# Kernel optimization log

Hardware: AMD Instinct MI355X
Metric: run time of the kernel (lower is better)

The kernel has to match this reference:

```python
import jax, jax.numpy as jnp
import numpy as np

EPS = 1e-6  # kernel_epsilon
NUM_HEADS = 16
NUM_SCALES = 3
ROPE_BASE = 10000.0


def _rope(x, base=ROPE_BASE):
    # x: [B, S, N, D]; rotary applied along seq dim 1 (RotaryPositionEmbedding.forward)
    B, S, N, D = x.shape
    inv_freq = 1.0 / (base ** (jnp.arange(0, D, 2, dtype=jnp.float32) / D))  # [D/2]
    t = jnp.arange(S, dtype=jnp.float32)
    freqs = t[:, None] * inv_freq[None, :]            # [S, D/2]
    emb = jnp.concatenate([freqs, freqs], axis=-1)    # [S, D]
    cos = jnp.cos(emb)[None, :, None, :]
    sin = jnp.sin(emb)[None, :, None, :]
    x1, x2 = jnp.split(x, 2, axis=-1)
    rot = jnp.concatenate([-x2, x1], axis=-1)         # rotate_half
    return x * cos + rot * sin


def _kernel(x):
    # elu kernel: F.elu(x) + 1.0 + epsilon
    return jax.nn.elu(x) + 1.0 + EPS


def setup_inputs() -> dict:
    key = jax.random.key(0)
    ks = jax.random.split(key, 12)
    B, S, H = 4, 2048, 1024
    sc = 1.0 / np.sqrt(H)
    inp = {
        "hidden_states": jax.random.normal(ks[0], (B, S, H), dtype=jnp.float32),
        "attention_mask": jnp.ones((B, S), dtype=jnp.float32),
        "Wq": jax.random.normal(ks[1], (H, H), dtype=jnp.float32) * sc,
        "bq": jnp.zeros((H,), dtype=jnp.float32),
        "Wk": jax.random.normal(ks[2], (H, H), dtype=jnp.float32) * sc,
        "bk": jnp.zeros((H,), dtype=jnp.float32),
        "Wv": jax.random.normal(ks[3], (H, H), dtype=jnp.float32) * sc,
        "bv": jnp.zeros((H,), dtype=jnp.float32),
        "Wo": jax.random.normal(ks[4], (H, H), dtype=jnp.float32) * sc,
        "bo": jnp.zeros((H,), dtype=jnp.float32),
        "Wg": jax.random.normal(ks[5], (H, 1), dtype=jnp.float32) * sc,
        "bg": jnp.zeros((1,), dtype=jnp.float32),  # gate_init_bias = 0.0
        "decay_factors": jnp.ones((NUM_SCALES,), dtype=jnp.float32) * 0.9,
        "gate_weights": jnp.ones((NUM_SCALES,), dtype=jnp.float32) / NUM_SCALES,
    }
    return inp


def reference(hidden_states, attention_mask, Wq, bq, Wk, bk, Wv, bv, Wo, bo,
              Wg, bg, decay_factors, gate_weights):
    B, S, H = hidden_states.shape
    N = NUM_HEADS
    D = H // N
    scaling = D ** -0.5

    q = (hidden_states @ Wq + bq).reshape(B, S, N, D)
    k = (hidden_states @ Wk + bk).reshape(B, S, N, D)
    v = (hidden_states @ Wv + bv).reshape(B, S, N, D)

    # rotary position embeddings on q, k
    q = _rope(q)
    k = _rope(k)

    # kernel feature maps (elu + 1 + eps), query scaling
    q = _kernel(q) * scaling
    k = _kernel(k)

    # apply padding mask to keys/values (mask.unsqueeze(-1).unsqueeze(-1))
    m = attention_mask[:, :, None, None]
    k = k * m
    v = v * m

    # linear (kernelized) attention over the sequence, fused form of
    # einsum('bsnk,bsnv->bsnkv').sum(dim=1)
    kv = jnp.einsum('bsnk,bsnv->bnkv', k, v)          # [B, N, D, D]
    k_sum = jnp.sum(k, axis=1)                        # [B, N, D]
    num = jnp.einsum('bsnk,bnkv->bsnv', q, kv)        # [B, S, N, D]
    den = jnp.einsum('bsnk,bnk->bsn', q, k_sum) + EPS
    attn_out = num / den[..., None]                   # [B, S, N, D]

    # multi-scale memory: starts at zero, one decayed update with this chunk
    decay_sig = jax.nn.sigmoid(decay_factors)                  # [M]
    memory = (1.0 - decay_sig)[None, :, None, None, None] * kv[:, None]  # [B,M,N,D,D]
    mem_scaled = jnp.einsum('bsnk,bmnkv->bmsnv', q, memory)    # [B,M,S,N,D]
    gate_soft = jax.nn.softmax(gate_weights, axis=0)           # [M]
    mem_out = jnp.sum(mem_scaled * gate_soft[None, :, None, None, None], axis=1)

    # sigmoid gate blending local linear attention with memory readout
    g = jax.nn.sigmoid(hidden_states @ Wg + bg)[..., None]     # [B, S, 1, 1]
    combined = g * attn_out + (1.0 - g) * mem_out              # [B, S, N, D]

    out = combined.reshape(B, S, H) @ Wo + bo
    return out
```

## Files before the change

### kernel.cpp

```cpp
#include <hip/hip_runtime.h>
#include <math.h>

#define B_   4
#define S_   2048
#define H_   1024
#define NH   16
#define HD   64
#define T_   (B_ * S_)
#define NCH  16

typedef unsigned short u16;
typedef __bf16 bf16x8 __attribute__((ext_vector_type(8)));
typedef float  f32x4  __attribute__((ext_vector_type(4)));

__device__ __forceinline__ float elu_k(float x) {
    return (x > 0.f ? x : (expf(x) - 1.f)) + 1.000001f;
}

__device__ __forceinline__ u16 f2bf(float x) {
    union { float f; unsigned int u; } v; v.f = x;
    unsigned int r = v.u + 0x7FFFu + ((v.u >> 16) & 1u);
    return (u16)(r >> 16);
}

__device__ __forceinline__ float bfl(unsigned int u) {
    union { unsigned int u; float f; } v; v.u = u << 16; return v.f;
}
__device__ __forceinline__ float bfh(unsigned int u) {
    union { unsigned int u; float f; } v; v.u = u & 0xFFFF0000u; return v.f;
}

__device__ __forceinline__ void async_load16(const u16* g, u16* l) {
    __builtin_amdgcn_global_load_lds(
        (const __attribute__((address_space(1))) void*)g,
        (__attribute__((address_space(3))) void*)l,
        16, 0, 0);
}

__global__ __launch_bounds__(256) void prep_kernel(
    const float* __restrict__ decay, const float* __restrict__ gate,
    float* __restrict__ coeff, float* __restrict__ cosT,
    float* __restrict__ sinT, const float* __restrict__ bq,
    const float* __restrict__ bk, const float* __restrict__ bv,
    float* __restrict__ bqkv) {
    int idx = blockIdx.x * 256 + threadIdx.x;
    if (idx < S_ * 32) {
        int s = idx >> 5, i = idx & 31;
        float inv = powf(10000.f, -(2.f * (float)i) / 64.f);
        float f = (float)s * inv;
        cosT[idx] = cosf(f);
        sinT[idx] = sinf(f);
    } else if (idx < S_ * 32 + 3072) {
        int i = idx - S_ * 32;
        bqkv[i] = (i < 1024) ? bq[i] : (i < 2048) ? bk[i - 1024] : bv[i - 2048];
    } else if (idx == S_ * 32 + 3072) {
        float g0 = gate[0], g1 = gate[1], g2 = gate[2];
        float mx = fmaxf(g0, fmaxf(g1, g2));
        float e0 = expf(g0 - mx), e1 = expf(g1 - mx), e2 = expf(g2 - mx);
        float inv = 1.f / (e0 + e1 + e2);
        float es[3] = {e0, e1, e2};
        float c = 0.f;
        for (int m = 0; m < 3; m++) {
            float ds = 1.f / (1.f + expf(-decay[m]));
            c += es[m] * inv * (1.f - ds);
        }
        *coeff = c;
    }
}

__global__ __launch_bounds__(256) void cvt_gate_kernel(
    const float* __restrict__ hs, const float* __restrict__ Wg,
    const float* __restrict__ bg, u16* __restrict__ hsb,
    float* __restrict__ gbuf) {
    int t = blockIdx.x;
    int i = threadIdx.x;
    float4 f = ((const float4*)(hs + (size_t)t * H_))[i];
    float4 w = ((const float4*)Wg)[i];
    ushort4 u;
    u.x = f2bf(f.x); u.y = f2bf(f.y); u.z = f2bf(f.z); u.w = f2bf(f.w);
    ((ushort4*)(hsb + (size_t)t * H_))[i] = u;
    float s = f.x * w.x + f.y * w.y + f.z * w.z + f.w * w.w;
#pragma unroll
    for (int off = 32; off > 0; off >>= 1) s += __shfl_down(s, off);
    __shared__ float wsum[4];
    if ((i & 63) == 0) wsum[i >> 6] = s;
    __syncthreads();
    if (i == 0) {
        float tot = wsum[0] + wsum[1] + wsum[2] + wsum[3];
        gbuf[t] = 1.f / (1.f + expf(-(tot + bg[0])));
    }
}

__global__ __launch_bounds__(256) void pack_w_kernel(
    const float* __restrict__ Wq, const float* __restrict__ Wk,
    const float* __restrict__ Wv, const float* __restrict__ Wo,
    u16* __restrict__ Wt) {
    __shared__ u16 tile[64][65];
    const float* W = (blockIdx.z == 0) ? Wq :
                     (blockIdx.z == 1) ? Wk :
                     (blockIdx.z == 2) ? Wv : Wo;
    int nt = blockIdx.x * 64, kt = blockIdx.y * 64;
    int tid = threadIdx.x;
#pragma unroll
    for (int it = 0; it < 16; it++) {
        int i = it * 256 + tid;
        int kr = i >> 6, nc = i & 63;
        tile[kr][nc] = f2bf(W[(size_t)(kt + kr) * H_ + nt + nc]);
    }
    __syncthreads();
    size_t wbase = (size_t)blockIdx.z * H_;
#pragma unroll
    for (int it = 0; it < 16; it++) {
        int i = it * 256 + tid;
        int nr = i >> 6, kc = i & 63;
        Wt[(wbase + nt + nr) * H_ + kt + kc] = tile[kc][nr];
    }
}

#define GEMM_KLOOP(A_, Bt_, bm_, bn_)                                         \
    for (int k0 = 0; k0 < K; k0 += 64) {                                      \
        _Pragma("unroll")                                                     \
        for (int h = 0; h < 2; h++) {                                         \
            _Pragma("unroll")                                                 \
            for (int i = 0; i < 2; i++) {                                     \
                int r0 = (wave * 2 + i) * 16;                                 \
                int rr = lane >> 2, cc = lane & 3;                            \
                async_load16(&A_[(size_t)(bm_ + r0 + rr) * K + k0 + h * 32 + cc * 8], \
                             &Asl[h][r0 * 32]);                               \
                async_load16(&Bt_[(size_t)(bn_ + r0 + rr) * K + k0 + h * 32 + cc * 8], \
                             &Bsl[h][r0 * 32]);                               \
            }                                                                 \
        }                                                                     \
        asm volatile("s_waitcnt vmcnt(0)" ::: "memory");                      \
        __syncthreads();                                                      \
        _Pragma("unroll")                                                     \
        for (int h = 0; h < 2; h++) {                                         \
            bf16x8 af[4], bfr[4];                                             \
            _Pragma("unroll")                                                 \
            for (int mi = 0; mi < 4; mi++)                                    \
                af[mi] = *(const bf16x8*)&Asl[h][(wm + mi * 16 + l15) * 32 + quad * 8]; \
            _Pragma("unroll")                                                 \
            for (int nj = 0; nj < 4; nj++)                                    \
                bfr[nj] = *(const bf16x8*)&Bsl[h][(wn + nj * 16 + l15) * 32 + quad * 8]; \
            _Pragma("unroll")                                                 \
            for (int mi = 0; mi < 4; mi++)                                    \
                _Pragma("unroll")                                             \
                for (int nj = 0; nj < 4; nj++)                                \
                    acc[mi][nj] = __builtin_amdgcn_mfma_f32_16x16x32_bf16(    \
                        af[mi], bfr[nj], acc[mi][nj], 0, 0, 0);               \
        }                                                                     \
        __syncthreads();                                                      \
    }

__global__ __launch_bounds__(256) void gemm_qkv_kernel(
    const u16* __restrict__ A, const u16* __restrict__ Bt,
    const float* __restrict__ bias, const float* __restrict__ mask,
    const float* __restrict__ cosT, const float* __restrict__ sinT,
    u16* __restrict__ qb, u16* __restrict__ kb, u16* __restrict__ vb) {
    constexpr int K = 1024;
    __shared__ u16 Asl[2][128 * 32];
    __shared__ u16 Bsl[2][128 * 32];
    const int tid  = threadIdx.x;
    const int wave = tid >> 6, lane = tid & 63;
    const int wm = (wave & 1) * 64, wn = (wave >> 1) * 64;
    const int bm = blockIdx.y * 128, bn = blockIdx.x * 128;
    const int l15 = lane & 15, quad = lane >> 4;

    f32x4 acc[4][4];
#pragma unroll
    for (int i = 0; i < 4; i++)
#pragma unroll
        for (int j = 0; j < 4; j++) acc[i][j] = {0.f, 0.f, 0.f, 0.f};

    GEMM_KLOOP(A, Bt, bm, bn)

    const int colbase = bn + wn;
    const int region  = colbase >> 10;
    const int n       = (colbase & 1023) >> 6;
    float bc[4];
#pragma unroll
    for (int nj = 0; nj < 4; nj++) bc[nj] = bias[colbase + nj * 16 + l15];
    u16* outp = (region == 0) ? qb : (region == 1) ? kb : vb;

#pragma unroll
    for (int mi = 0; mi < 4; mi++) {
#pragma unroll
        for (int r = 0; r < 4; r++) {
            int row = bm + wm + mi * 16 + quad * 4 + r;
            int b = row >> 11, s = row & (S_ - 1);
            size_t obase = ((size_t)(b * 16 + n) * S_ + s) * 64;
            if (region < 2) {
                float mfac = (region == 0) ? 0.125f : mask[row];
#pragma unroll
                for (int p = 0; p < 2; p++) {
                    int d1 = p * 16 + l15;
                    float c  = cosT[s * 32 + d1];
                    float sn = sinT[s * 32 + d1];
                    float x1 = acc[mi][p][r]     + bc[p];
                    float x2 = acc[mi][p + 2][r] + bc[p + 2];
                    float r1 = x1 * c - x2 * sn;
                    float r2 = x2 * c + x1 * sn;
                    outp[obase + d1]      = f2bf(elu_k(r1) * mfac);
                    outp[obase + d1 + 32] = f2bf(elu_k(r2) * mfac);
                }
            } else {
                float mfac = mask[row];
#pragma unroll
                for (int nj = 0; nj < 4; nj++)
                    outp[obase + nj * 16 + l15] =
                        f2bf((acc[mi][nj][r] + bc[nj]) * mfac);
            }
        }
    }
}

__global__ __launch_bounds__(256) void gemm_out_kernel(
    const u16* __restrict__ A, const u16* __restrict__ Bt,
    const float* __restrict__ bias, float* __restrict__ C, int N) {
    constexpr int K = 1024;
    __shared__ u16 Asl[2][128 * 32];
    __shared__ u16 Bsl[2][128 * 32];
    const int tid  = threadIdx.x;
    const int wave = tid >> 6, lane = tid & 63;
    const int wm = (wave & 1) * 64, wn = (wave >> 1) * 64;
    const int bm = blockIdx.y * 128, bn = blockIdx.x * 128;
    const int l15 = lane & 15, quad = lane >> 4;

    f32x4 acc[4][4];
#pragma unroll
    for (int i = 0; i < 4; i++)
#pragma unroll
        for (int j = 0; j < 4; j++) acc[i][j] = {0.f, 0.f, 0.f, 0.f};

    GEMM_KLOOP(A, Bt, bm, bn)

#pragma unroll
    for (int mi = 0; mi < 4; mi++) {
#pragma unroll
        for (int nj = 0; nj < 4; nj++) {
            int col = bn + wn + nj * 16 + l15;
            float bcol = bias[col];
#pragma unroll
            for (int r = 0; r < 4; r++) {
                int row = bm + wm + mi * 16 + quad * 4 + r;
                C[(size_t)row * N + col] = acc[mi][nj][r] + bcol;
            }
        }
    }
}

__global__ __launch_bounds__(256) void kv_part_kernel(
    const u16* __restrict__ kb, const u16* __restrict__ vb,
    float* __restrict__ kvpart, float* __restrict__ kspart) {
    int bn = blockIdx.x;
    const int rows = S_ / NCH;
    int s0 = blockIdx.y * rows;
    int tid = threadIdx.x;
    int ti = tid >> 4, tj = tid & 15;
    __shared__ float ks[16][64], vs[16][64];
    float acc[4][4] = {};
    float ksacc = 0.f;
    const u16* kbase = kb + (size_t)bn * (S_ * 64) + (size_t)s0 * 64;
    const u16* vbase = vb + (size_t)bn * (S_ * 64) + (size_t)s0 * 64;
    for (int ss = 0; ss < rows; ss += 16) {
        {
            int half = tid >> 7;
            int c = tid & 127;
            int rr = c >> 3, col = (c & 7) * 8;
            const u16* src = (half ? vbase : kbase) + (size_t)(ss + rr) * 64 + col;
            uint4 raw = *(const uint4*)src;
            float* dst = half ? &vs[rr][col] : &ks[rr][col];
            dst[0] = bfl(raw.x); dst[1] = bfh(raw.x);
            dst[2] = bfl(raw.y); dst[3] = bfh(raw.y);
            dst[4] = bfl(raw.z); dst[5] = bfh(raw.z);
            dst[6] = bfl(raw.w); dst[7] = bfh(raw.w);
        }
        __syncthreads();
#pragma unroll
        for (int r = 0; r < 16; r++) {
            float a[4], bb[4];
#pragma unroll
            for (int i = 0; i < 4; i++) a[i] = ks[r][ti * 4 + i];
#pragma unroll
            for (int j = 0; j < 4; j++) bb[j] = vs[r][tj * 4 + j];
#pragma unroll
            for (int i = 0; i < 4; i++)
#pragma unroll
                for (int j = 0; j < 4; j++)
                    acc[i][j] = fmaf(a[i], bb[j], acc[i][j]);
        }
        if (tid < 64) {
#pragma unroll
            for (int r = 0; r < 16; r++) ksacc += ks[r][tid];
        }
        __syncthreads();
    }
    size_t obase = ((size_t)blockIdx.y * 64 + bn) * 4096;
#pragma unroll
    for (int i = 0; i < 4; i++)
#pragma unroll
        for (int j = 0; j < 4; j++)
            kvpart[obase + (size_t)(ti * 4 + i) * 64 + tj * 4 + j] = acc[i][j];
    if (tid < 64)
        kspart[((size_t)blockIdx.y * 64 + bn) * 64 + tid] = ksacc;
}

__global__ __launch_bounds__(256) void reduce_part_kernel(
    const float* __restrict__ kvpart, const float* __restrict__ kspart,
    float* __restrict__ kvb, float* __restrict__ ksum) {
    int i = blockIdx.x * 256 + threadIdx.x;
    if (i < 262144) {
        float s = 0.f;
#pragma unroll
        for (int c = 0; c < NCH; c++) s += kvpart[(size_t)c * 262144 + i];
        kvb[i] = s;
    } else if (i < 262144 + 4096) {
        int j = i - 262144;
        float s = 0.f;
#pragma unroll
        for (int c = 0; c < NCH; c++) s += kspart[(size_t)c * 4096 + j];
        ksum[j] = s;
    }
}

__global__ __launch_bounds__(256) void combine_kernel(
    const u16* __restrict__ qb, const float* __restrict__ kvb,
    const float* __restrict__ ksum, const float* __restrict__ g,
    const float* __restrict__ coeffp, u16* __restrict__ cmb) {
    int bn = blockIdx.x;
    int b = bn >> 4, n = bn & 15;
    __shared__ u16 qs[256 * 72];
    __shared__ u16 kvT[64 * 72];
    __shared__ u16 ksl[128];
    int tid = threadIdx.x;
    int s0 = blockIdx.y * 256;

    const u16* qsrc = qb + (size_t)bn * (S_ * 64) + (size_t)s0 * 64;
    for (int c = tid; c < 2048; c += 256) {
        int t = c >> 3, k8 = (c & 7) * 8;
        float4 tmp = *(const float4*)(qsrc + (size_t)c * 8);
        *(float4*)&qs[t * 72 + k8] = tmp;
    }
    for (int c = tid; c < 1024; c += 256) {
        int i = c >> 4, d4 = (c & 15) * 4;
        float4 kvv = *(const float4*)&kvb[(size_t)bn * 4096 + i * 64 + d4];
        kvT[(d4 + 0) * 72 + i] = f2bf(kvv.x);
        kvT[(d4 + 1) * 72 + i] = f2bf(kvv.y);
        kvT[(d4 + 2) * 72 + i] = f2bf(kvv.z);
        kvT[(d4 + 3) * 72 + i] = f2bf(kvv.w);
    }
    if (tid < 64)        ksl[tid] = f2bf(ksum[bn * 64 + tid]);
    else if (tid < 128)  ksl[tid] = 0;
    __syncthreads();

    int wave = tid >> 6, lane = tid & 63;
    int l15 = lane & 15, quad = lane >> 4;
    int wt = wave * 64;

    int ko0 = (l15 == 0) ? quad * 8      : 64;
    int ko1 = (l15 == 0) ? 32 + quad * 8 : 64;
    bf16x8 ksf0 = *(const bf16x8*)&ksl[ko0];
    bf16x8 ksf1 = *(const bf16x8*)&ksl[ko1];

    bf16x8 bfr0[4], bfr1[4];
#pragma unroll
    for (int nj = 0; nj < 4; nj++) {
        bfr0[nj] = *(const bf16x8*)&kvT[(nj * 16 + l15) * 72 + quad * 8];
        bfr1[nj] = *(const bf16x8*)&kvT[(nj * 16 + l15) * 72 + 32 + quad * 8];
    }

    f32x4 acc[4][4], dacc[4];
#pragma unroll
    for (int i = 0; i < 4; i++) {
        dacc[i] = {0.f, 0.f, 0.f, 0.f};
#pragma unroll
        for (int j = 0; j < 4; j++) acc[i][j] = {0.f, 0.f, 0.f, 0.f};
    }

#pragma unroll
    for (int mi = 0; mi < 4; mi++) {
        bf16x8 a0 = *(const bf16x8*)&qs[(wt + mi * 16 + l15) * 72 + quad * 8];
        bf16x8 a1 = *(const bf16x8*)&qs[(wt + mi * 16 + l15) * 72 + 32 + quad * 8];
        dacc[mi] = __builtin_amdgcn_mfma_f32_16x16x32_bf16(a0, ksf0, dacc[mi], 0, 0, 0);
        dacc[mi] = __builtin_amdgcn_mfma_f32_16x16x32_bf16(a1, ksf1, dacc[mi], 0, 0, 0);
#pragma unroll
        for (int nj = 0; nj < 4; nj++) {
            acc[mi][nj] = __builtin_amdgcn_mfma_f32_16x16x32_bf16(
                a0, bfr0[nj], acc[mi][nj], 0, 0, 0);
            acc[mi][nj] = __builtin_amdgcn_mfma_f32_16x16x32_bf16(
                a1, bfr1[nj], acc[mi][nj], 0, 0, 0);
        }
    }

    float coeff = *coeffp;
#pragma unroll
    for (int mi = 0; mi < 4; mi++) {
#pragma unroll
        for (int r = 0; r < 4; r++) {
            int s = s0 + wt + mi * 16 + quad * 4 + r;
            int t = b * S_ + s;
            float den = __shfl(dacc[mi][r], lane & 48) + 1e-6f;
            float gv = g[t];
            float w1 = gv / den + (1.f - gv) * coeff;
#pragma unroll
            for (int nj = 0; nj < 4; nj++) {
                int d = nj * 16 + l15;
                cmb[(size_t)t * H_ + n * 64 + d] = f2bf(acc[mi][nj][r] * w1);
            }
        }
    }
}

extern "C" void kernel_launch(void* const* d_in, const int* in_sizes, int n_in,
                              void* d_out, int out_size, void* d_ws, size_t ws_size,
                              hipStream_t stream) {
    const float* hs    = (const float*)d_in[0];
    const float* mask  = (const float*)d_in[1];
    const float* Wq    = (const float*)d_in[2];
    const float* bq    = (const float*)d_in[3];
    const float* Wk    = (const float*)d_in[4];
    const float* bk    = (const float*)d_in[5];
    const float* Wv    = (const float*)d_in[6];
    const float* bv    = (const float*)d_in[7];
    const float* Wo    = (const float*)d_in[8];
    const float* bo    = (const float*)d_in[9];
    const float* Wg    = (const float*)d_in[10];
    const float* bg    = (const float*)d_in[11];
    const float* decay = (const float*)d_in[12];
    const float* gate  = (const float*)d_in[13];
    float* out = (float*)d_out;

    float* ws     = (float*)d_ws;
    float* kvb    = ws;
    float* ksum   = kvb + 262144;
    float* gbuf   = ksum + 4096;
    float* coeff  = gbuf + 8192;
    float* cosT   = coeff + 64;
    float* sinT   = cosT + 65536;
    float* bqkv   = sinT + 65536;
    float* kspart = bqkv + 4096;
    float* kvpart = kspart + 65536;
    u16*   hsb    = (u16*)(kvpart + 4194304);
    u16*   Wt     = hsb + (size_t)T_ * H_;
    u16*   WoT    = Wt + (size_t)3072 * H_;
    u16*   qb     = Wt + (size_t)4096 * H_;
    u16*   kb     = qb + (size_t)T_ * H_;
    u16*   vb     = kb + (size_t)T_ * H_;
    u16*   cmb    = vb + (size_t)T_ * H_;

    prep_kernel<<<(S_ * 32 + 3072 + 256) / 256 + 1, 256, 0, stream>>>(
        decay, gate, coeff, cosT, sinT, bq, bk, bv, bqkv);
    cvt_gate_kernel<<<T_, 256, 0, stream>>>(hs, Wg, bg, hsb, gbuf);
    pack_w_kernel<<<dim3(16, 16, 4), 256, 0, stream>>>(Wq, Wk, Wv, Wo, Wt);

    gemm_qkv_kernel<<<dim3(3072 / 128, T_ / 128), 256, 0, stream>>>(
        hsb, Wt, bqkv, mask, cosT, sinT, qb, kb, vb);

    kv_part_kernel<<<dim3(B_ * NH, NCH), 256, 0, stream>>>(
        kb, vb, kvpart, kspart);
    reduce_part_kernel<<<(262144 + 4096 + 255) / 256, 256, 0, stream>>>(
        kvpart, kspart, kvb, ksum);

    combine_kernel<<<dim3(B_ * NH, S_ / 256), 256, 0, stream>>>(
        qb, kvb, ksum, gbuf, coeff, cmb);

    gemm_out_kernel<<<dim3(H_ / 128, T_ / 128), 256, 0, stream>>>(
        cmb, WoT, bo, out, H_);
}
```

Before: 272.5 us.

## Enlarge GEMM block tile to 256x128 with K-step 32 and merge prologue kernels

Both GEMM kernels now use a 256x128 block tile, with each wave computing 128x64 and the K loop stepping by 32 instead of 64. Each B fragment is reused across eight A fragments, which raises arithmetic intensity per LDS load, and launch bounds request two blocks per CU. The bf16 conversion and gate kernel is merged with the prep kernel into one launch to save a kernel launch. The cost is more accumulator registers, half as many blocks, and twice as many barrier-synchronized K iterations, each with fewer MFMAs per wave.

```diff
diff --git a/kernel.cpp b/kernel.cpp
--- a/kernel.cpp
+++ b/kernel.cpp
@@ -37,13 +37,36 @@
         16, 0, 0);
 }
 
-__global__ __launch_bounds__(256) void prep_kernel(
+__global__ __launch_bounds__(256) void prologue_kernel(
+    const float* __restrict__ hs, const float* __restrict__ Wg,
+    const float* __restrict__ bg, u16* __restrict__ hsb,
+    float* __restrict__ gbuf,
     const float* __restrict__ decay, const float* __restrict__ gate,
     float* __restrict__ coeff, float* __restrict__ cosT,
     float* __restrict__ sinT, const float* __restrict__ bq,
     const float* __restrict__ bk, const float* __restrict__ bv,
     float* __restrict__ bqkv) {
-    int idx = blockIdx.x * 256 + threadIdx.x;
+    if (blockIdx.x < T_) {
+        int t = blockIdx.x;
+        int i = threadIdx.x;
+        float4 f = ((const float4*)(hs + (size_t)t * H_))[i];
+        float4 w = ((const float4*)Wg)[i];
+        ushort4 u;
+        u.x = f2bf(f.x); u.y = f2bf(f.y); u.z = f2bf(f.z); u.w = f2bf(f.w);
+        ((ushort4*)(hsb + (size_t)t * H_))[i] = u;
+        float s = f.x * w.x + f.y * w.y + f.z * w.z + f.w * w.w;
+#pragma unroll
+        for (int off = 32; off > 0; off >>= 1) s += __shfl_down(s, off);
+        __shared__ float wsum[4];
+        if ((i & 63) == 0) wsum[i >> 6] = s;
+        __syncthreads();
+        if (i == 0) {
+            float tot = wsum[0] + wsum[1] + wsum[2] + wsum[3];
+            gbuf[t] = 1.f / (1.f + expf(-(tot + bg[0])));
+        }
+        return;
+    }
+    int idx = (blockIdx.x - T_) * 256 + threadIdx.x;
     if (idx < S_ * 32) {
         int s = idx >> 5, i = idx & 31;
         float inv = powf(10000.f, -(2.f * (float)i) / 64.f);
@@ -68,29 +91,6 @@
     }
 }
 
-__global__ __launch_bounds__(256) void cvt_gate_kernel(
-    const float* __restrict__ hs, const float* __restrict__ Wg,
-    const float* __restrict__ bg, u16* __restrict__ hsb,
-    float* __restrict__ gbuf) {
-    int t = blockIdx.x;
-    int i = threadIdx.x;
-    float4 f = ((const float4*)(hs + (size_t)t * H_))[i];
-    float4 w = ((const float4*)Wg)[i];
-    ushort4 u;
-    u.x = f2bf(f.x); u.y = f2bf(f.y); u.z = f2bf(f.z); u.w = f2bf(f.w);
-    ((ushort4*)(hsb + (size_t)t * H_))[i] = u;
-    float s = f.x * w.x + f.y * w.y + f.z * w.z + f.w * w.w;
-#pragma unroll
-    for (int off = 32; off > 0; off >>= 1) s += __shfl_down(s, off);
-    __shared__ float wsum[4];
-    if ((i & 63) == 0) wsum[i >> 6] = s;
-    __syncthreads();
-    if (i == 0) {
-        float tot = wsum[0] + wsum[1] + wsum[2] + wsum[3];
-        gbuf[t] = 1.f / (1.f + expf(-(tot + bg[0])));
-    }
-}
-
 __global__ __launch_bounds__(256) void pack_w_kernel(
     const float* __restrict__ Wq, const float* __restrict__ Wk,
     const float* __restrict__ Wv, const float* __restrict__ Wo,
@@ -118,57 +118,53 @@
 }
 
 #define GEMM_KLOOP(A_, Bt_, bm_, bn_)                                         \
-    for (int k0 = 0; k0 < K; k0 += 64) {                                      \
+    for (int k0 = 0; k0 < K; k0 += 32) {                                      \
         _Pragma("unroll")                                                     \
-        for (int h = 0; h < 2; h++) {                                         \
-            _Pragma("unroll")                                                 \
-            for (int i = 0; i < 2; i++) {                                     \
-                int r0 = (wave * 2 + i) * 16;                                 \
-                int rr = lane >> 2, cc = lane & 3;                            \
-                async_load16(&A_[(size_t)(bm_ + r0 + rr) * K + k0 + h * 32 + cc * 8], \
-                             &Asl[h][r0 * 32]);                               \
-                async_load16(&Bt_[(size_t)(bn_ + r0 + rr) * K + k0 + h * 32 + cc * 8], \
-                             &Bsl[h][r0 * 32]);                               \
-            }                                                                 \
+        for (int i = 0; i < 4; i++) {                                         \
+            int r0 = wave * 64 + i * 16;                                      \
+            async_load16(&A_[(size_t)(bm_ + r0 + (lane >> 2)) * K + k0 + (lane & 3) * 8], \
+                         &Asl[r0 * 32]);                                      \
+        }                                                                     \
+        _Pragma("unroll")                                                     \
+        for (int i = 0; i < 2; i++) {                                         \
+            int r0 = wave * 32 + i * 16;                                      \
+            async_load16(&Bt_[(size_t)(bn_ + r0 + (lane >> 2)) * K + k0 + (lane & 3) * 8], \
+                         &Bsl[r0 * 32]);                                      \
         }                                                                     \
         asm volatile("s_waitcnt vmcnt(0)" ::: "memory");                      \
         __syncthreads();                                                      \
+        bf16x8 bfr[4];                                                        \
         _Pragma("unroll")                                                     \
-        for (int h = 0; h < 2; h++) {                                         \
-            bf16x8 af[4], bfr[4];                                             \
-            _Pragma("unroll")                                                 \
-            for (int mi = 0; mi < 4; mi++)                                    \
-                af[mi] = *(const bf16x8*)&Asl[h][(wm + mi * 16 + l15) * 32 + quad * 8]; \
+        for (int nj = 0; nj < 4; nj++)                                        \
+            bfr[nj] = *(const bf16x8*)&Bsl[(wn + nj * 16 + l15) * 32 + quad * 8]; \
+        _Pragma("unroll")                                                     \
+        for (int mi = 0; mi < 8; mi++) {                                      \
+            bf16x8 a = *(const bf16x8*)&Asl[(wm + mi * 16 + l15) * 32 + quad * 8]; \
             _Pragma("unroll")                                                 \
             for (int nj = 0; nj < 4; nj++)                                    \
-                bfr[nj] = *(const bf16x8*)&Bsl[h][(wn + nj * 16 + l15) * 32 + quad * 8]; \
-            _Pragma("unroll")                                                 \
-            for (int mi = 0; mi < 4; mi++)                                    \
-                _Pragma("unroll")                                             \
-                for (int nj = 0; nj < 4; nj++)                                \
-                    acc[mi][nj] = __builtin_amdgcn_mfma_f32_16x16x32_bf16(    \
-                        af[mi], bfr[nj], acc[mi][nj], 0, 0, 0);               \
+                acc[mi][nj] = __builtin_amdgcn_mfma_f32_16x16x32_bf16(        \
+                    a, bfr[nj], acc[mi][nj], 0, 0, 0);                        \
         }                                                                     \
         __syncthreads();                                                      \
     }
 
-__global__ __launch_bounds__(256) void gemm_qkv_kernel(
+__global__ __launch_bounds__(256, 2) void gemm_qkv_kernel(
     const u16* __restrict__ A, const u16* __restrict__ Bt,
     const float* __restrict__ bias, const float* __restrict__ mask,
     const float* __restrict__ cosT, const float* __restrict__ sinT,
     u16* __restrict__ qb, u16* __restrict__ kb, u16* __restrict__ vb) {
     constexpr int K = 1024;
-    __shared__ u16 Asl[2][128 * 32];
-    __shared__ u16 Bsl[2][128 * 32];
+    __shared__ u16 Asl[256 * 32];
+    __shared__ u16 Bsl[128 * 32];
     const int tid  = threadIdx.x;
     const int wave = tid >> 6, lane = tid & 63;
-    const int wm = (wave & 1) * 64, wn = (wave >> 1) * 64;
-    const int bm = blockIdx.y * 128, bn = blockIdx.x * 128;
+    const int wm = (wave & 1) * 128, wn = (wave >> 1) * 64;
+    const int bm = blockIdx.y * 256, bn = blockIdx.x * 128;
     const int l15 = lane & 15, quad = lane >> 4;
 
-    f32x4 acc[4][4];
-#pragma unroll
-    for (int i = 0; i < 4; i++)
+    f32x4 acc[8][4];
+#pragma unroll
+    for (int i = 0; i < 8; i++)
 #pragma unroll
         for (int j = 0; j < 4; j++) acc[i][j] = {0.f, 0.f, 0.f, 0.f};
 
@@ -183,7 +179,7 @@
     u16* outp = (region == 0) ? qb : (region == 1) ? kb : vb;
 
 #pragma unroll
-    for (int mi = 0; mi < 4; mi++) {
+    for (int mi = 0; mi < 8; mi++) {
 #pragma unroll
         for (int r = 0; r < 4; r++) {
             int row = bm + wm + mi * 16 + quad * 4 + r;
@@ -214,28 +210,28 @@
     }
 }
 
-__global__ __launch_bounds__(256) void gemm_out_kernel(
+__global__ __launch_bounds__(256, 2) void gemm_out_kernel(
     const u16* __restrict__ A, const u16* __restrict__ Bt,
     const float* __restrict__ bias, float* __restrict__ C, int N) {
     constexpr int K = 1024;
-    __shared__ u16 Asl[2][128 * 32];
-    __shared__ u16 Bsl[2][128 * 32];
+    __shared__ u16 Asl[256 * 32];
+    __shared__ u16 Bsl[128 * 32];
     const int tid  = threadIdx.x;
     const int wave = tid >> 6, lane = tid & 63;
-    const int wm = (wave & 1) * 64, wn = (wave >> 1) * 64;
-    const int bm = blockIdx.y * 128, bn = blockIdx.x * 128;
+    const int wm = (wave & 1) * 128, wn = (wave >> 1) * 64;
+    const int bm = blockIdx.y * 256, bn = blockIdx.x * 128;
     const int l15 = lane & 15, quad = lane >> 4;
 
-    f32x4 acc[4][4];
-#pragma unroll
-    for (int i = 0; i < 4; i++)
+    f32x4 acc[8][4];
+#pragma unroll
+    for (int i = 0; i < 8; i++)
 #pragma unroll
         for (int j = 0; j < 4; j++) acc[i][j] = {0.f, 0.f, 0.f, 0.f};
 
     GEMM_KLOOP(A, Bt, bm, bn)
 
 #pragma unroll
-    for (int mi = 0; mi < 4; mi++) {
+    for (int mi = 0; mi < 8; mi++) {
 #pragma unroll
         for (int nj = 0; nj < 4; nj++) {
             int col = bn + wn + nj * 16 + l15;
@@ -448,12 +444,11 @@
     u16*   vb     = kb + (size_t)T_ * H_;
     u16*   cmb    = vb + (size_t)T_ * H_;
 
-    prep_kernel<<<(S_ * 32 + 3072 + 256) / 256 + 1, 256, 0, stream>>>(
-        decay, gate, coeff, cosT, sinT, bq, bk, bv, bqkv);
-    cvt_gate_kernel<<<T_, 256, 0, stream>>>(hs, Wg, bg, hsb, gbuf);
+    prologue_kernel<<<T_ + (S_ * 32 + 3072 + 256) / 256 + 1, 256, 0, stream>>>(
+        hs, Wg, bg, hsb, gbuf, decay, gate, coeff, cosT, sinT, bq, bk, bv, bqkv);
     pack_w_kernel<<<dim3(16, 16, 4), 256, 0, stream>>>(Wq, Wk, Wv, Wo, Wt);
 
-    gemm_qkv_kernel<<<dim3(3072 / 128, T_ / 128), 256, 0, stream>>>(
+    gemm_qkv_kernel<<<dim3(3072 / 128, T_ / 256), 256, 0, stream>>>(
         hsb, Wt, bqkv, mask, cosT, sinT, qb, kb, vb);
 
     kv_part_kernel<<<dim3(B_ * NH, NCH), 256, 0, stream>>>(
@@ -464,6 +459,6 @@
     combine_kernel<<<dim3(B_ * NH, S_ / 256), 256, 0, stream>>>(
         qb, kvb, ksum, gbuf, coeff, cmb);
 
-    gemm_out_kernel<<<dim3(H_ / 128, T_ / 128), 256, 0, stream>>>(
+    gemm_out_kernel<<<dim3(H_ / 128, T_ / 256), 256, 0, stream>>>(
         cmb, WoT, bo, out, H_);
 }
```

Result: slower. 292.0 us (+7.2%).

## Merge prologue kernels and replace KV partial reduction with atomics

Applied to the files above, without the earlier changes.

Folds the three setup kernels (rope tables and misc, bf16 convert plus gate, weight pack) into one prologue kernel that dispatches on block index. The same prologue also zeroes the kv/ksum accumulators. The KV partial kernel then atomically adds its chunk results into those accumulators, which removes the separate reduce kernel and the 16 MB partial buffer round-trip. Launch count and memory traffic drop, at the cost of atomic contention (16 chunks per element) and non-deterministic summation order.

```diff
diff --git a/kernel.cpp b/kernel.cpp
--- a/kernel.cpp
+++ b/kernel.cpp
@@ -9,6 +9,12 @@
 #define T_   (B_ * S_)
 #define NCH  16
 
+#define PB_CVT   T_
+#define PB_PACK  1024
+#define PB_ROPE  256
+#define PB_MISC  13
+#define PB_ZERO  260
+
 typedef unsigned short u16;
 typedef __bf16 bf16x8 __attribute__((ext_vector_type(8)));
 typedef float  f32x4  __attribute__((ext_vector_type(4)));
@@ -37,84 +43,97 @@
         16, 0, 0);
 }
 
-__global__ __launch_bounds__(256) void prep_kernel(
+__global__ __launch_bounds__(256) void prologue_kernel(
+    const float* __restrict__ hs, const float* __restrict__ Wg,
+    const float* __restrict__ bg, u16* __restrict__ hsb,
+    float* __restrict__ gbuf,
+    const float* __restrict__ Wq, const float* __restrict__ Wk,
+    const float* __restrict__ Wv, const float* __restrict__ Wo,
+    u16* __restrict__ Wt,
     const float* __restrict__ decay, const float* __restrict__ gate,
     float* __restrict__ coeff, float* __restrict__ cosT,
     float* __restrict__ sinT, const float* __restrict__ bq,
     const float* __restrict__ bk, const float* __restrict__ bv,
-    float* __restrict__ bqkv) {
-    int idx = blockIdx.x * 256 + threadIdx.x;
-    if (idx < S_ * 32) {
+    float* __restrict__ bqkv, float* __restrict__ zbase) {
+    __shared__ u16 tile[64][65];
+    __shared__ float wsum[4];
+    int bi = blockIdx.x;
+    int tid = threadIdx.x;
+
+    if (bi < PB_CVT) {
+        int t = bi;
+        float4 f = ((const float4*)(hs + (size_t)t * H_))[tid];
+        float4 w = ((const float4*)Wg)[tid];
+        ushort4 u;
+        u.x = f2bf(f.x); u.y = f2bf(f.y); u.z = f2bf(f.z); u.w = f2bf(f.w);
+        ((ushort4*)(hsb + (size_t)t * H_))[tid] = u;
+        float s = f.x * w.x + f.y * w.y + f.z * w.z + f.w * w.w;
+#pragma unroll
+        for (int off = 32; off > 0; off >>= 1) s += __shfl_down(s, off);
+        if ((tid & 63) == 0) wsum[tid >> 6] = s;
+        __syncthreads();
+        if (tid == 0) {
+            float tot = wsum[0] + wsum[1] + wsum[2] + wsum[3];
+            gbuf[t] = 1.f / (1.f + expf(-(tot + bg[0])));
+        }
+        return;
+    }
+    bi -= PB_CVT;
+    if (bi < PB_PACK) {
+        int wsel = bi >> 8;
+        int kt = ((bi >> 4) & 15) * 64, nt = (bi & 15) * 64;
+        const float* W = (wsel == 0) ? Wq : (wsel == 1) ? Wk :
+                         (wsel == 2) ? Wv : Wo;
+#pragma unroll
+        for (int it = 0; it < 16; it++) {
+            int i = it * 256 + tid;
+            int kr = i >> 6, nc = i & 63;
+            tile[kr][nc] = f2bf(W[(size_t)(kt + kr) * H_ + nt + nc]);
+        }
+        __syncthreads();
+        size_t wbase = (size_t)wsel * H_;
+#pragma unroll
+        for (int it = 0; it < 16; it++) {
+            int i = it * 256 + tid;
+            int nr = i >> 6, kc = i & 63;
+            Wt[(wbase + nt + nr) * H_ + kt + kc] = tile[kc][nr];
+        }
+        return;
+    }
+    bi -= PB_PACK;
+    if (bi < PB_ROPE) {
+        int idx = bi * 256 + tid;
         int s = idx >> 5, i = idx & 31;
         float inv = powf(10000.f, -(2.f * (float)i) / 64.f);
         float f = (float)s * inv;
         cosT[idx] = cosf(f);
         sinT[idx] = sinf(f);
-    } else if (idx < S_ * 32 + 3072) {
-        int i = idx - S_ * 32;
-        bqkv[i] = (i < 1024) ? bq[i] : (i < 2048) ? bk[i - 1024] : bv[i - 2048];
-    } else if (idx == S_ * 32 + 3072) {
-        float g0 = gate[0], g1 = gate[1], g2 = gate[2];
-        float mx = fmaxf(g0, fmaxf(g1, g2));
-        float e0 = expf(g0 - mx), e1 = expf(g1 - mx), e2 = expf(g2 - mx);
-        float inv = 1.f / (e0 + e1 + e2);
-        float es[3] = {e0, e1, e2};
-        float c = 0.f;
-        for (int m = 0; m < 3; m++) {
-            float ds = 1.f / (1.f + expf(-decay[m]));
-            c += es[m] * inv * (1.f - ds);
-        }
-        *coeff = c;
-    }
-}
-
-__global__ __launch_bounds__(256) void cvt_gate_kernel(
-    const float* __restrict__ hs, const float* __restrict__ Wg,
-    const float* __restrict__ bg, u16* __restrict__ hsb,
-    float* __restrict__ gbuf) {
-    int t = blockIdx.x;
-    int i = threadIdx.x;
-    float4 f = ((const float4*)(hs + (size_t)t * H_))[i];
-    float4 w = ((const float4*)Wg)[i];
-    ushort4 u;
-    u.x = f2bf(f.x); u.y = f2bf(f.y); u.z = f2bf(f.z); u.w = f2bf(f.w);
-    ((ushort4*)(hsb + (size_t)t * H_))[i] = u;
-    float s = f.x * w.x + f.y * w.y + f.z * w.z + f.w * w.w;
-#pragma unroll
-    for (int off = 32; off > 0; off >>= 1) s += __shfl_down(s, off);
-    __shared__ float wsum[4];
-    if ((i & 63) == 0) wsum[i >> 6] = s;
-    __syncthreads();
-    if (i == 0) {
-        float tot = wsum[0] + wsum[1] + wsum[2] + wsum[3];
-        gbuf[t] = 1.f / (1.f + expf(-(tot + bg[0])));
-    }
-}
-
-__global__ __launch_bounds__(256) void pack_w_kernel(
-    const float* __restrict__ Wq, const float* __restrict__ Wk,
-    const float* __restrict__ Wv, const float* __restrict__ Wo,
-    u16* __restrict__ Wt) {
-    __shared__ u16 tile[64][65];
-    const float* W = (blockIdx.z == 0) ? Wq :
-                     (blockIdx.z == 1) ? Wk :
-                     (blockIdx.z == 2) ? Wv : Wo;
-    int nt = blockIdx.x * 64, kt = blockIdx.y * 64;
-    int tid = threadIdx.x;
-#pragma unroll
-    for (int it = 0; it < 16; it++) {
-        int i = it * 256 + tid;
-        int kr = i >> 6, nc = i & 63;
-        tile[kr][nc] = f2bf(W[(size_t)(kt + kr) * H_ + nt + nc]);
-    }
-    __syncthreads();
-    size_t wbase = (size_t)blockIdx.z * H_;
-#pragma unroll
-    for (int it = 0; it < 16; it++) {
-        int i = it * 256 + tid;
-        int nr = i >> 6, kc = i & 63;
-        Wt[(wbase + nt + nr) * H_ + kt + kc] = tile[kc][nr];
-    }
+        return;
+    }
+    bi -= PB_ROPE;
+    if (bi < PB_MISC) {
+        int i = bi * 256 + tid;
+        if (i < 3072) {
+            bqkv[i] = (i < 1024) ? bq[i] : (i < 2048) ? bk[i - 1024]
+                                                      : bv[i - 2048];
+        } else if (i == 3072) {
+            float g0 = gate[0], g1 = gate[1], g2 = gate[2];
+            float mx = fmaxf(g0, fmaxf(g1, g2));
+            float e0 = expf(g0 - mx), e1 = expf(g1 - mx), e2 = expf(g2 - mx);
+            float inv = 1.f / (e0 + e1 + e2);
+            float es[3] = {e0, e1, e2};
+            float c = 0.f;
+            for (int m = 0; m < 3; m++) {
+                float ds = 1.f / (1.f + expf(-decay[m]));
+                c += es[m] * inv * (1.f - ds);
+            }
+            *coeff = c;
+        }
+        return;
+    }
+    bi -= PB_MISC;
+    int i = bi * 256 + tid;
+    if (i < 66560) ((float4*)zbase)[i] = {0.f, 0.f, 0.f, 0.f};
 }
 
 #define GEMM_KLOOP(A_, Bt_, bm_, bn_)                                         \
@@ -251,7 +270,7 @@
 
 __global__ __launch_bounds__(256) void kv_part_kernel(
     const u16* __restrict__ kb, const u16* __restrict__ vb,
-    float* __restrict__ kvpart, float* __restrict__ kspart) {
+    float* __restrict__ kvb, float* __restrict__ ksum) {
     int bn = blockIdx.x;
     const int rows = S_ / NCH;
     int s0 = blockIdx.y * rows;
@@ -295,32 +314,13 @@
         }
         __syncthreads();
     }
-    size_t obase = ((size_t)blockIdx.y * 64 + bn) * 4096;
 #pragma unroll
     for (int i = 0; i < 4; i++)
 #pragma unroll
         for (int j = 0; j < 4; j++)
-            kvpart[obase + (size_t)(ti * 4 + i) * 64 + tj * 4 + j] = acc[i][j];
-    if (tid < 64)
-        kspart[((size_t)blockIdx.y * 64 + bn) * 64 + tid] = ksacc;
-}
-
-__global__ __launch_bounds__(256) void reduce_part_kernel(
-    const float* __restrict__ kvpart, const float* __restrict__ kspart,
-    float* __restrict__ kvb, float* __restrict__ ksum) {
-    int i = blockIdx.x * 256 + threadIdx.x;
-    if (i < 262144) {
-        float s = 0.f;
-#pragma unroll
-        for (int c = 0; c < NCH; c++) s += kvpart[(size_t)c * 262144 + i];
-        kvb[i] = s;
-    } else if (i < 262144 + 4096) {
-        int j = i - 262144;
-        float s = 0.f;
-#pragma unroll
-        for (int c = 0; c < NCH; c++) s += kspart[(size_t)c * 4096 + j];
-        ksum[j] = s;
-    }
+            atomicAdd(&kvb[(size_t)bn * 4096 + (size_t)(ti * 4 + i) * 64 + tj * 4 + j],
+                      acc[i][j]);
+    if (tid < 64) atomicAdd(&ksum[bn * 64 + tid], ksacc);
 }
 
 __global__ __launch_bounds__(256) void combine_kernel(
@@ -438,9 +438,7 @@
     float* cosT   = coeff + 64;
     float* sinT   = cosT + 65536;
     float* bqkv   = sinT + 65536;
-    float* kspart = bqkv + 4096;
-    float* kvpart = kspart + 65536;
-    u16*   hsb    = (u16*)(kvpart + 4194304);
+    u16*   hsb    = (u16*)(bqkv + 4096);
     u16*   Wt     = hsb + (size_t)T_ * H_;
     u16*   WoT    = Wt + (size_t)3072 * H_;
     u16*   qb     = Wt + (size_t)4096 * H_;
@@ -448,18 +446,16 @@
     u16*   vb     = kb + (size_t)T_ * H_;
     u16*   cmb    = vb + (size_t)T_ * H_;
 
-    prep_kernel<<<(S_ * 32 + 3072 + 256) / 256 + 1, 256, 0, stream>>>(
-        decay, gate, coeff, cosT, sinT, bq, bk, bv, bqkv);
-    cvt_gate_kernel<<<T_, 256, 0, stream>>>(hs, Wg, bg, hsb, gbuf);
-    pack_w_kernel<<<dim3(16, 16, 4), 256, 0, stream>>>(Wq, Wk, Wv, Wo, Wt);
+    const int pgrid = PB_CVT + PB_PACK + PB_ROPE + PB_MISC + PB_ZERO;
+    prologue_kernel<<<pgrid, 256, 0, stream>>>(
+        hs, Wg, bg, hsb, gbuf, Wq, Wk, Wv, Wo, Wt,
+        decay, gate, coeff, cosT, sinT, bq, bk, bv, bqkv, kvb);
 
     gemm_qkv_kernel<<<dim3(3072 / 128, T_ / 128), 256, 0, stream>>>(
         hsb, Wt, bqkv, mask, cosT, sinT, qb, kb, vb);
 
     kv_part_kernel<<<dim3(B_ * NH, NCH), 256, 0, stream>>>(
-        kb, vb, kvpart, kspart);
-    reduce_part_kernel<<<(262144 + 4096 + 255) / 256, 256, 0, stream>>>(
-        kvpart, kspart, kvb, ksum);
+        kb, vb, kvb, ksum);
 
     combine_kernel<<<dim3(B_ * NH, S_ / 256), 256, 0, stream>>>(
         qb, kvb, ksum, gbuf, coeff, cmb);
```

New measurement: 311.5 us. +14.3%, slower.
